# Optimization experiments

Hardware: AMD Instinct MI355X
Metric: run time of the kernel (lower is better)

## Reference

```python
import jax, jax.numpy as jnp
import numpy as np

V = 50257; CTX = 2048; D = 1024; H = 16; L = 8; DH = D // H
B = 2; S = 2048; EPS = 1e-5


def setup_inputs() -> dict:
    key = jax.random.key(0)
    ks = jax.random.split(key, 8)
    s = 0.02
    def n(k, shape):
        return jax.random.normal(k, shape, jnp.float32) * s
    return {
        "x": jax.random.randint(ks[0], (B, S), 0, V),
        "wte": n(ks[1], (V, D)),
        "wpe": n(ks[2], (CTX, D)),
        "ln1_g": jnp.ones((L, D), jnp.float32), "ln1_b": jnp.zeros((L, D), jnp.float32),
        "w_qkv": n(ks[3], (L, D, 3 * D)), "b_qkv": jnp.zeros((L, 3 * D), jnp.float32),
        "w_proj": n(ks[4], (L, D, D)), "b_proj": jnp.zeros((L, D), jnp.float32),
        "ln2_g": jnp.ones((L, D), jnp.float32), "ln2_b": jnp.zeros((L, D), jnp.float32),
        "w_fc": n(ks[5], (L, D, 4 * D)), "b_fc": jnp.zeros((L, 4 * D), jnp.float32),
        "w_cp": n(ks[6], (L, 4 * D, D)), "b_cp": jnp.zeros((L, D), jnp.float32),
        "lnf_g": jnp.ones((D,), jnp.float32), "lnf_b": jnp.zeros((D,), jnp.float32),
        "w_head": n(ks[7], (D, V)),
    }


def layernorm(x, g, b):
    m = x.mean(-1, keepdims=True)
    v = ((x - m) ** 2).mean(-1, keepdims=True)
    return (x - m) * jax.lax.rsqrt(v + EPS) * g + b


def gpt_forward(x, wte, wpe, ln1_g, ln1_b, w_qkv, b_qkv, w_proj, b_proj,
                ln2_g, ln2_b, w_fc, b_fc, w_cp, b_cp, lnf_g, lnf_b, w_head):
    Bx, Sx = x.shape
    h = wte[x] + wpe[:Sx]                       # [B,S,D]
    mask = jnp.tril(jnp.ones((Sx, Sx), bool))   # causal mask
    scale = DH ** -0.5

    def block(h, p):
        g1, b1, wq, bq, wp, bp, g2, b2, wf, bf, wc, bc = p
        y = layernorm(h, g1, b1)
        qkv = y @ wq + bq                        # [B,S,3D]
        q, k, v = jnp.split(qkv, 3, axis=-1)
        q = q.reshape(Bx, Sx, H, DH)
        k = k.reshape(Bx, Sx, H, DH)
        v = v.reshape(Bx, Sx, H, DH)
        att = jnp.einsum('bqhd,bkhd->bhqk', q, k) * scale
        att = jnp.where(mask, att, -jnp.inf)
        att = jax.nn.softmax(att, axis=-1)
        z = jnp.einsum('bhqk,bkhd->bqhd', att, v).reshape(Bx, Sx, D)
        h = h + z @ wp + bp
        y2 = layernorm(h, g2, b2)
        h = h + jax.nn.gelu(y2 @ wf + bf, approximate=False) @ wc + bc
        return h, None

    h, _ = jax.lax.scan(block, h, (ln1_g, ln1_b, w_qkv, b_qkv, w_proj, b_proj,
                                   ln2_g, ln2_b, w_fc, b_fc, w_cp, b_cp))
    h = layernorm(h, lnf_g, lnf_b)
    logits = h[:, -1:, :] @ w_head              # [B,1,V] (last position only)
    return logits


def reference(x, wte, wpe, ln1_g, ln1_b, w_qkv, b_qkv, w_proj, b_proj,
              ln2_g, ln2_b, w_fc, b_fc, w_cp, b_cp, lnf_g, lnf_b, w_head):
    return gpt_forward(x, wte, wpe, ln1_g, ln1_b, w_qkv, b_qkv, w_proj, b_proj,
                       ln2_g, ln2_b, w_fc, b_fc, w_cp, b_cp, lnf_g, lnf_b, w_head)
```

## Files before the change

### kernel.cpp

```cpp
#include <hip/hip_runtime.h>
#include <hip/hip_bf16.h>
#include <math.h>

#define VOCAB 50257
#define CTX 2048
#define DMODEL 1024
#define NHEAD 16
#define NLAYER 8
#define DHEAD 64
#define BATCH 2
#define SEQ 2048
#define NTOK (BATCH * SEQ)

typedef __bf16 bf16x8 __attribute__((ext_vector_type(8)));
typedef float  f32x4  __attribute__((ext_vector_type(4)));
typedef unsigned short ushort4v __attribute__((ext_vector_type(4)));
typedef unsigned short ushort8v __attribute__((ext_vector_type(8)));

__device__ inline void gl_lds16(const void* g, void* l) {
    __builtin_amdgcn_global_load_lds(
        (const __attribute__((address_space(1))) unsigned int*)g,
        (__attribute__((address_space(3))) unsigned int*)l, 16, 0, 0);
}

__device__ inline unsigned short f2bs(float v) {
    __hip_bfloat16 t = __float2bfloat16(v);
    return *(unsigned short*)&t;
}

__global__ void embed_kernel(const int* __restrict__ x,
                             const float* __restrict__ wte,
                             const float* __restrict__ wpe,
                             float* __restrict__ h) {
    int t = blockIdx.x;
    int s = t & (SEQ - 1);
    int tok = x[t];
    const float* pe = wpe + (long)s * DMODEL;
    const float* te = wte + (long)tok * DMODEL;
    float* ph = h + (long)t * DMODEL;
    for (int d = threadIdx.x; d < DMODEL; d += 256)
        ph[d] = te[d] + pe[d];
}

__device__ inline float wave_sum(float v) {
    for (int off = 32; off; off >>= 1) v += __shfl_xor(v, off);
    return v;
}

__device__ void ln_body(char* smem, int row, const float* __restrict__ in,
                        unsigned short* __restrict__ out,
                        const float* __restrict__ g, const float* __restrict__ b) {
    float* red  = (float*)smem;
    float* red2 = red + 4;
    const float* px = in + (long)row * DMODEL;
    unsigned short* po = out + (long)row * DMODEL;
    int tid = threadIdx.x;
    int wid = tid >> 6, lane = tid & 63;

    float x[4];
    float s = 0.f;
    #pragma unroll
    for (int i = 0; i < 4; ++i) { x[i] = px[tid + i * 256]; s += x[i]; }
    s = wave_sum(s);
    if (lane == 0) red[wid] = s;
    __syncthreads();
    float mean = (red[0] + red[1] + red[2] + red[3]) * (1.0f / DMODEL);

    float s2 = 0.f;
    #pragma unroll
    for (int i = 0; i < 4; ++i) { float d = x[i] - mean; s2 += d * d; }
    s2 = wave_sum(s2);
    if (lane == 0) red2[wid] = s2;
    __syncthreads();
    float var = (red2[0] + red2[1] + red2[2] + red2[3]) * (1.0f / DMODEL);
    float r = 1.0f / sqrtf(var + 1e-5f);
    #pragma unroll
    for (int i = 0; i < 4; ++i) {
        int d = tid + i * 256;
        po[d] = f2bs((x[i] - mean) * r * g[d] + b[d]);
    }
}

__global__ void ln_final(const float* __restrict__ in, float* __restrict__ out,
                         const float* __restrict__ g, const float* __restrict__ b,
                         long row_stride) {
    __shared__ float red[4], red2[4];
    int row = blockIdx.x;
    const float* px = in + (long)row * row_stride;
    float* po = out + (long)row * DMODEL;
    int tid = threadIdx.x;
    int wid = tid >> 6, lane = tid & 63;
    float x[4];
    float s = 0.f;
    #pragma unroll
    for (int i = 0; i < 4; ++i) { x[i] = px[tid + i * 256]; s += x[i]; }
    s = wave_sum(s);
    if (lane == 0) red[wid] = s;
    __syncthreads();
    float mean = (red[0] + red[1] + red[2] + red[3]) * (1.0f / DMODEL);
    float s2 = 0.f;
    #pragma unroll
    for (int i = 0; i < 4; ++i) { float d = x[i] - mean; s2 += d * d; }
    s2 = wave_sum(s2);
    if (lane == 0) red2[wid] = s2;
    __syncthreads();
    float var = (red2[0] + red2[1] + red2[2] + red2[3]) * (1.0f / DMODEL);
    float r = 1.0f / sqrtf(var + 1e-5f);
    #pragma unroll
    for (int i = 0; i < 4; ++i) {
        int d = tid + i * 256;
        po[d] = (x[i] - mean) * r * g[d] + b[d];
    }
}

__device__ void convT_body(char* smem, int kx, int ny, const float* __restrict__ W,
                           unsigned short* __restrict__ WT, int K, int N) {
    float (*t)[65] = (float(*)[65])smem;
    const int k0 = kx * 64, n0 = ny * 64;
    const int tid = threadIdx.x;
    {
        const int krow = tid >> 4, c4 = (tid & 15) * 4;
        #pragma unroll
        for (int p = 0; p < 4; ++p) {
            f32x4 gv = *(const f32x4*)&W[(long)(k0 + p * 16 + krow) * N + n0 + c4];
            #pragma unroll
            for (int j = 0; j < 4; ++j) t[p * 16 + krow][c4 + j] = gv[j];
        }
    }
    __syncthreads();
    {
        const int n = tid >> 3, kl = (tid & 7) * 8;
        #pragma unroll
        for (int p = 0; p < 2; ++p) {
            ushort8v pk;
            #pragma unroll
            for (int j = 0; j < 8; ++j) pk[j] = f2bs(t[kl + j][p * 32 + n]);
            *(ushort8v*)&WT[(long)(n0 + p * 32 + n) * K + k0 + kl] = pk;
        }
    }
}

#define STG_A(KS, H) do { \
    const unsigned short* g_ = A + (long)(bm + (H) * 128 + srow) * K + (KS) * 64 + stgch; \
    unsigned short* s_ = LDS + (((KS) & 1) * 2 + (H)) * 8192 + (w * 8) * 64; \
    gl_lds16(g_, s_); gl_lds16(g_ + 64L * K, s_ + 4096); \
} while (0)
#define STG_B(KS, H) do { \
    const unsigned short* g_ = BT + (long)(bn + (H) * 128 + srow) * K + (KS) * 64 + stgch; \
    unsigned short* s_ = LDS + 32768 + (((KS) & 1) * 2 + (H)) * 8192 + (w * 8) * 64; \
    gl_lds16(g_, s_); gl_lds16(g_ + 64L * K, s_ + 4096); \
} while (0)
#define MM2(M_, x0, x1) do { \
    acc[M_][0] = __builtin_amdgcn_mfma_f32_16x16x32_bf16(x0, bfr[0], acc[M_][0], 0, 0, 0); \
    acc[M_][0] = __builtin_amdgcn_mfma_f32_16x16x32_bf16(x1, bfr[1], acc[M_][0], 0, 0, 0); \
    acc[M_][1] = __builtin_amdgcn_mfma_f32_16x16x32_bf16(x0, bfr[2], acc[M_][1], 0, 0, 0); \
    acc[M_][1] = __builtin_amdgcn_mfma_f32_16x16x32_bf16(x1, bfr[3], acc[M_][1], 0, 0, 0); \
    acc[M_][2] = __builtin_amdgcn_mfma_f32_16x16x32_bf16(x0, bfr[4], acc[M_][2], 0, 0, 0); \
    acc[M_][2] = __builtin_amdgcn_mfma_f32_16x16x32_bf16(x1, bfr[5], acc[M_][2], 0, 0, 0); \
    acc[M_][3] = __builtin_amdgcn_mfma_f32_16x16x32_bf16(x0, bfr[6], acc[M_][3], 0, 0, 0); \
    acc[M_][3] = __builtin_amdgcn_mfma_f32_16x16x32_bf16(x1, bfr[7], acc[M_][3], 0, 0, 0); \
} while (0)
#define PHASE(Q, SPAR, STAGE_STMT, TAIL_STMT) do { \
    bf16x8 a00, a01, a10, a11; \
    if (((Q) & 3) == 0) { \
        const unsigned short* Bb_ = lBp[SPAR] + ((wc & 1) * 64 + fr) * 64; \
        bfr[0] = *(const bf16x8*)(Bb_ + rd0);        bfr[1] = *(const bf16x8*)(Bb_ + rd1); \
        bfr[2] = *(const bf16x8*)(Bb_ + 1024 + rd0); bfr[3] = *(const bf16x8*)(Bb_ + 1024 + rd1); \
        bfr[4] = *(const bf16x8*)(Bb_ + 2048 + rd0); bfr[5] = *(const bf16x8*)(Bb_ + 2048 + rd1); \
        bfr[6] = *(const bf16x8*)(Bb_ + 3072 + rd0); bfr[7] = *(const bf16x8*)(Bb_ + 3072 + rd1); \
    } \
    { const unsigned short* Ab_ = lAp[SPAR] + fr * 64; \
      a00 = *(const bf16x8*)(Ab_ + (((Q) & 3) * 2) * 1024 + rd0); \
      a01 = *(const bf16x8*)(Ab_ + (((Q) & 3) * 2) * 1024 + rd1); \
      a10 = *(const bf16x8*)(Ab_ + (((Q) & 3) * 2 + 1) * 1024 + rd0); \
      a11 = *(const bf16x8*)(Ab_ + (((Q) & 3) * 2 + 1) * 1024 + rd1); } \
    STAGE_STMT; \
    __builtin_amdgcn_s_barrier(); \
    asm volatile("s_waitcnt lgkmcnt(0)" ::: "memory"); \
    __builtin_amdgcn_sched_barrier(0); \
    __builtin_amdgcn_s_setprio(1); \
    MM2(((Q) & 3) * 2, a00, a01); \
    MM2(((Q) & 3) * 2 + 1, a10, a11); \
    __builtin_amdgcn_s_setprio(0); \
    TAIL_STMT; \
    __builtin_amdgcn_s_barrier(); \
} while (0)

template<int EPI>
__global__ __launch_bounds__(512, 1)
void mm_mfma256(const unsigned short* __restrict__ A,
                const unsigned short* __restrict__ BT,
                const float* __restrict__ bias,
                void* __restrict__ Cout, int M, int N, int K, int nbx) {
    extern __shared__ unsigned short LDS[];
    const int tid = threadIdx.x;
    const int w = tid >> 6, lane = tid & 63;
    const int wr = w >> 2, wc = w & 3;
    const int nwg = gridDim.x, bid = blockIdx.x;
    const int swz = (bid & 7) * (nwg >> 3) + (bid >> 3);
    const int bm = (swz / nbx) * 256, bn = (swz % nbx) * 256;

    f32x4 acc[8][4];
    #pragma unroll
    for (int m = 0; m < 8; ++m)
        #pragma unroll
        for (int n = 0; n < 4; ++n)
            acc[m][n] = (f32x4){0.f, 0.f, 0.f, 0.f};

    const int fr = lane & 15, kg = lane >> 4;
    const int rd0 = 8 * (kg ^ (lane & 7)), rd1 = 8 * ((kg + 4) ^ (lane & 7));
    const int stgch = 8 * ((lane & 7) ^ (lane >> 3));
    const int srow = w * 8 + (lane >> 3);
    unsigned short* const lAp[2] = { LDS + wr * 8192, LDS + (2 + wr) * 8192 };
    unsigned short* const lBp[2] = { LDS + 32768 + (wc >> 1) * 8192,
                                     LDS + 32768 + (2 + (wc >> 1)) * 8192 };
    bf16x8 bfr[8];

    STG_B(0, 0); STG_B(0, 1); STG_A(0, 0); STG_A(0, 1); STG_B(1, 0); STG_B(1, 1);
    asm volatile("s_waitcnt vmcnt(4)" ::: "memory");
    __builtin_amdgcn_sched_barrier(0);
    __builtin_amdgcn_s_barrier();

    const int T = K >> 7;
    for (int t = 0; t < T; ++t) {
        const int s = 2 * t;
        const bool nl = (t < T - 1);
        PHASE(0, 0, STG_A(s + 1, 0), );
        PHASE(1, 0, STG_A(s + 1, 1), );
        PHASE(2, 0, if (nl) STG_B(s + 2, 0), );
        PHASE(3, 0, if (nl) STG_B(s + 2, 1),
              if (nl) { asm volatile("s_waitcnt vmcnt(4)" ::: "memory"); } else { asm volatile("s_waitcnt vmcnt(0)" ::: "memory"); } __builtin_amdgcn_sched_barrier(0); );
        PHASE(4, 1, if (nl) STG_A(s + 2, 0), );
        PHASE(5, 1, if (nl) STG_A(s + 2, 1), );
        PHASE(6, 1, if (nl) STG_B(s + 3, 0), );
        PHASE(7, 1, if (nl) STG_B(s + 3, 1),
              if (nl) { asm volatile("s_waitcnt vmcnt(4)" ::: "memory"); __builtin_amdgcn_sched_barrier(0); } );
    }

    const int r0 = (lane >> 4) * 4;
    #pragma unroll
    for (int n = 0; n < 4; ++n) {
        int colb = bn + wc * 64 + n * 16;
        float bv = bias[colb + fr];
        #pragma unroll
        for (int m = 0; m < 8; ++m) {
            int rowb = bm + wr * 128 + m * 16 + r0;
            if (EPI == 3) {
                unsigned short* qkvB = (unsigned short*)Cout;
                int which = colb >> 10, hh = (colb & 1023) >> 6, dbase = colb & 63;
                int b_ = rowb >> 11, s_ = rowb & 2047;
                long bh2 = b_ * 16 + hh;
                float v[4];
                #pragma unroll
                for (int r = 0; r < 4; ++r) v[r] = acc[m][n][r] + bv;
                if (which == 2) {
                    ushort4v pk;
                    #pragma unroll
                    for (int r = 0; r < 4; ++r) pk[r] = f2bs(v[r]);
                    *(ushort4v*)&qkvB[8388608L + (bh2 * 64 + dbase + fr) * 2048 + s_] = pk;
                } else {
                    unsigned short* dst = qkvB + (long)which * 4194304L +
                                          (bh2 * 2048 + s_) * 64 + dbase + fr;
                    #pragma unroll
                    for (int r = 0; r < 4; ++r) dst[r * 64] = f2bs(v[r]);
                }
            } else {
                #pragma unroll
                for (int r = 0; r < 4; ++r) {
                    long row = rowb + r, col = colb + fr;
                    float v = acc[m][n][r] + bv;
                    v = 0.5f * v * (1.0f + erff(v * 0.70710678118f));
                    ((__hip_bfloat16*)Cout)[row * N + col] = __float2bfloat16(v);
                }
            }
        }
    }
}

__global__ __launch_bounds__(256)
void mm_mfma_n64(const unsigned short* __restrict__ A,
                 const unsigned short* __restrict__ BT,
                 const float* __restrict__ bias, const float* __restrict__ R,
                 float* __restrict__ Cout, int M, int N, int K) {
    __shared__ unsigned short As[2][128 * 32];
    __shared__ unsigned short Bs[2][64 * 32];
    const int tid = threadIdx.x;
    const int w = tid >> 6, lane = tid & 63;
    const int bm = blockIdx.y * 128, bn = blockIdx.x * 64;
    const int wr = (w >> 1) * 64, wc = (w & 1) * 32;

    f32x4 acc[4][2];
    #pragma unroll
    for (int m = 0; m < 4; ++m)
        #pragma unroll
        for (int n = 0; n < 2; ++n)
            acc[m][n] = (f32x4){0.f, 0.f, 0.f, 0.f};

    const int lrow = lane >> 2;
    const int lcol = (lane & 3) * 8;
    const unsigned short* gA = A + (long)(bm + w * 32 + lrow) * K + lcol;
    const unsigned short* gB = BT + (long)(bn + w * 16 + lrow) * K + lcol;

#define N64_STAGE(K0, BB) do { \
    gl_lds16(gA + (K0),          &As[BB][(w * 32) * 32]); \
    gl_lds16(gA + (K0) + 16 * K, &As[BB][(w * 32 + 16) * 32]); \
    gl_lds16(gB + (K0),          &Bs[BB][(w * 16) * 32]); \
} while (0)

    N64_STAGE(0, 0);
    asm volatile("s_waitcnt vmcnt(0)" ::: "memory");
    __builtin_amdgcn_sched_barrier(0);
    __builtin_amdgcn_s_barrier();

    const int T = K >> 5;
    for (int t = 0; t < T; ++t) {
        const int buf = t & 1;
        if (t + 1 < T) N64_STAGE((t + 1) * 32, buf ^ 1);

        bf16x8 a[4], b[2];
        #pragma unroll
        for (int m = 0; m < 4; ++m)
            a[m] = *(const bf16x8*)&As[buf][(wr + m * 16 + (lane & 15)) * 32 + (lane >> 4) * 8];
        #pragma unroll
        for (int n = 0; n < 2; ++n)
            b[n] = *(const bf16x8*)&Bs[buf][(wc + n * 16 + (lane & 15)) * 32 + (lane >> 4) * 8];
        #pragma unroll
        for (int m = 0; m < 4; ++m)
            #pragma unroll
            for (int n = 0; n < 2; ++n)
                acc[m][n] = __builtin_amdgcn_mfma_f32_16x16x32_bf16(a[m], b[n], acc[m][n], 0, 0, 0);

        asm volatile("s_waitcnt vmcnt(0)" ::: "memory");
        __builtin_amdgcn_sched_barrier(0);
        __builtin_amdgcn_s_barrier();
    }
#undef N64_STAGE

    const int r0 = (lane >> 4) * 4, cc = lane & 15;
    #pragma unroll
    for (int n = 0; n < 2; ++n) {
        int colb = bn + wc + n * 16;
        float bv = bias[colb + cc];
        #pragma unroll
        for (int m = 0; m < 4; ++m) {
            int rowb = bm + wr + m * 16 + r0;
            #pragma unroll
            for (int r = 0; r < 4; ++r) {
                long row = rowb + r, col = colb + cc;
                float v = acc[m][n][r] + bv + R[row * N + col];
                Cout[row * N + col] = v;
            }
        }
    }
}

__device__ void attn_body(char* smem, int bh, int qb,
                          const unsigned short* __restrict__ qB,
                          const unsigned short* __restrict__ kB,
                          const unsigned short* __restrict__ vT,
                          __hip_bfloat16* __restrict__ z) {
    const int tid = threadIdx.x, w = tid >> 6, lane = tid & 63;
    const int arow = lane & 15, kg = lane >> 4;
    unsigned short* Ks = (unsigned short*)smem;
    unsigned short* Vs = Ks + 128 * 64;
    unsigned short* Ps = Vs + 64 * 128 + w * 16 * 128;

    const long kvbase = (long)bh * (2048 * 64);

    bf16x8 qa[2];
    {
        const unsigned short* q0 = qB + kvbase + (long)(qb + w * 16 + arow) * 64 + kg * 8;
        qa[0] = *(const bf16x8*)(q0);
        qa[1] = *(const bf16x8*)(q0 + 32);
    }

    f32x4 po[4];
    float mrow[4], lrow[4];
    #pragma unroll
    for (int i = 0; i < 4; ++i) {
        po[i] = (f32x4){0.f, 0.f, 0.f, 0.f};
        mrow[i] = -1e30f; lrow[i] = 0.f;
    }

    const int ksrow = lane >> 3;
    const int kschunk = (lane & 7) ^ ksrow;
    const int vsr = lane >> 4;
    const int cmax = qb >> 7;

    for (int c = 0; c <= cmax; ++c) {
        {
            const unsigned short* ks0 = kB + kvbase +
                (long)(c * 128 + w * 32 + ksrow) * 64 + kschunk * 8;
            #pragma unroll
            for (int i = 0; i < 4; ++i)
                gl_lds16(ks0 + (long)i * 8 * 64, &Ks[(w * 32 + i * 8) * 64]);
            #pragma unroll
            for (int i = 0; i < 4; ++i) {
                int d = w * 16 + i * 4 + vsr;
                int sch = (lane & 15) ^ (d & 7);
                gl_lds16(vT + kvbase + (long)d * 2048 + c * 128 + sch * 8,
                         &Vs[(w * 16 + i * 4) * 128]);
            }
        }
        __syncthreads();

        f32x4 s[8];
        #pragma unroll
        for (int n = 0; n < 8; ++n) {
            s[n] = (f32x4){0.f, 0.f, 0.f, 0.f};
            int row = n * 16 + arow, sw = row & 7;
            bf16x8 kb0 = *(const bf16x8*)&Ks[row * 64 + (kg ^ sw) * 8];
            bf16x8 kb1 = *(const bf16x8*)&Ks[row * 64 + ((4 + kg) ^ sw) * 8];
            s[n] = __builtin_amdgcn_mfma_f32_16x16x32_bf16(qa[0], kb0, s[n], 0, 0, 0);
            s[n] = __builtin_amdgcn_mfma_f32_16x16x32_bf16(qa[1], kb1, s[n], 0, 0, 0);
        }

        const bool diag = (c == cmax);
        #pragma unroll
        for (int n = 0; n < 8; ++n)
            #pragma unroll
            for (int r = 0; r < 4; ++r) {
                float v = s[n][r] * 0.125f;
                if (diag) {
                    int key = c * 128 + n * 16 + arow;
                    int qrow = qb + w * 16 + kg * 4 + r;
                    if (key > qrow) v = -1e30f;
                }
                s[n][r] = v;
            }

        #pragma unroll
        for (int r = 0; r < 4; ++r) {
            float rm = s[0][r];
            #pragma unroll
            for (int n = 1; n < 8; ++n) rm = fmaxf(rm, s[n][r]);
            #pragma unroll
            for (int off = 1; off < 16; off <<= 1)
                rm = fmaxf(rm, __shfl_xor(rm, off));
            float mnew = fmaxf(mrow[r], rm);
            float esc = expf(mrow[r] - mnew);
            float rs = 0.f;
            #pragma unroll
            for (int n = 0; n < 8; ++n) {
                float p = expf(s[n][r] - mnew);
                s[n][r] = p;
                rs += p;
            }
            #pragma unroll
            for (int off = 1; off < 16; off <<= 1)
                rs += __shfl_xor(rs, off);
            lrow[r] = lrow[r] * esc + rs;
            #pragma unroll
            for (int dt = 0; dt < 4; ++dt) po[dt][r] *= esc;
            mrow[r] = mnew;
        }

        #pragma unroll
        for (int n = 0; n < 8; ++n) {
            int col = n * 16 + arow;
            int chunk = col >> 3, cw = col & 7;
            #pragma unroll
            for (int r = 0; r < 4; ++r) {
                int row = kg * 4 + r;
                Ps[row * 128 + ((chunk ^ (row & 7)) * 8 + cw)] = f2bs(s[n][r]);
            }
        }

        bf16x8 pa[4];
        #pragma unroll
        for (int ks = 0; ks < 4; ++ks)
            pa[ks] = *(const bf16x8*)&Ps[arow * 128 + (((ks * 4 + kg) ^ (arow & 7)) * 8)];
        #pragma unroll
        for (int dt = 0; dt < 4; ++dt) {
            int vrow = dt * 16 + arow, sw = vrow & 7;
            #pragma unroll
            for (int ks = 0; ks < 4; ++ks) {
                bf16x8 vb = *(const bf16x8*)&Vs[vrow * 128 + (((ks * 4 + kg) ^ sw) * 8)];
                po[dt] = __builtin_amdgcn_mfma_f32_16x16x32_bf16(pa[ks], vb, po[dt], 0, 0, 0);
            }
        }
        __syncthreads();
    }

    const int b_ = bh >> 4, hofs = (bh & 15) * 64;
    #pragma unroll
    for (int dt = 0; dt < 4; ++dt)
        #pragma unroll
        for (int r = 0; r < 4; ++r) {
            long row = (long)b_ * 2048 + qb + w * 16 + kg * 4 + r;
            z[row * 1024 + hofs + dt * 16 + arow] = __float2bfloat16(po[dt][r] / lrow[r]);
        }
}

__global__ __launch_bounds__(256)
void fused_ln_convT(const float* __restrict__ h, unsigned short* __restrict__ y,
                    const float* __restrict__ g, const float* __restrict__ b,
                    const float* __restrict__ W, unsigned short* __restrict__ WT,
                    int K, int N, int nLN) {
    extern __shared__ char smem[];
    int bid = blockIdx.x;
    if (bid < nLN) {
        ln_body(smem, bid, h, y, g, b);
    } else {
        int r = bid - nLN, kt = K >> 6;
        convT_body(smem, r % kt, r / kt, W, WT, K, N);
    }
}

__global__ __launch_bounds__(256)
void fused_attn_convT2(const unsigned short* __restrict__ qB,
                       const unsigned short* __restrict__ kB,
                       const unsigned short* __restrict__ vT,
                       __hip_bfloat16* __restrict__ z,
                       const float* __restrict__ W1, unsigned short* __restrict__ WT1,
                       int K1, int N1, int n1,
                       const float* __restrict__ W2, unsigned short* __restrict__ WT2,
                       int K2, int N2, int nAttn) {
    extern __shared__ char smem[];
    int bid = blockIdx.x;
    if (bid < nAttn) {
        attn_body(smem, bid & 31, (bid >> 5) * 64, qB, kB, vT, z);
    } else if (bid < nAttn + n1) {
        int r = bid - nAttn, kt = K1 >> 6;
        convT_body(smem, r % kt, r / kt, W1, WT1, K1, N1);
    } else {
        int r = bid - nAttn - n1, kt = K2 >> 6;
        convT_body(smem, r % kt, r / kt, W2, WT2, K2, N2);
    }
}

__global__ void head_kernel(const float* __restrict__ hl, const float* __restrict__ W,
                            float* __restrict__ out) {
    __shared__ float hs[2 * DMODEL];
    int tid = threadIdx.x;
    #pragma unroll
    for (int i = 0; i < 8; ++i) hs[tid + i * 256] = hl[tid + i * 256];
    __syncthreads();
    int v = blockIdx.x * 256 + tid;
    if (v >= VOCAB) return;
    float a0 = 0.f, a1 = 0.f;
    for (int d = 0; d < DMODEL; ++d) {
        float wv = W[(long)d * VOCAB + v];
        a0 += hs[d] * wv;
        a1 += hs[DMODEL + d] * wv;
    }
    out[v] = a0;
    out[VOCAB + v] = a1;
}

extern "C" void kernel_launch(void* const* d_in, const int* in_sizes, int n_in,
                              void* d_out, int out_size, void* d_ws, size_t ws_size,
                              hipStream_t stream) {
    const int*   x      = (const int*)  d_in[0];
    const float* wte    = (const float*)d_in[1];
    const float* wpe    = (const float*)d_in[2];
    const float* ln1_g  = (const float*)d_in[3];
    const float* ln1_b  = (const float*)d_in[4];
    const float* w_qkv  = (const float*)d_in[5];
    const float* b_qkv  = (const float*)d_in[6];
    const float* w_proj = (const float*)d_in[7];
    const float* b_proj = (const float*)d_in[8];
    const float* ln2_g  = (const float*)d_in[9];
    const float* ln2_b  = (const float*)d_in[10];
    const float* w_fc   = (const float*)d_in[11];
    const float* b_fc   = (const float*)d_in[12];
    const float* w_cp   = (const float*)d_in[13];
    const float* b_cp   = (const float*)d_in[14];
    const float* lnf_g  = (const float*)d_in[15];
    const float* lnf_b  = (const float*)d_in[16];
    const float* w_head = (const float*)d_in[17];
    float* out = (float*)d_out;

    char* ws = (char*)d_ws;
    float*          h     = (float*)ws;
    unsigned short* qkvB  = (unsigned short*)(ws + (16L << 20));
    unsigned short* y_bf  = (unsigned short*)(ws + (40L << 20));
    __hip_bfloat16* z_bf  = (__hip_bfloat16*)(ws + (48L << 20));
    unsigned short* fc_bf = (unsigned short*)(ws + (56L << 20));
    unsigned short* wT_a  = (unsigned short*)(ws + (88L << 20));
    unsigned short* wT_b  = (unsigned short*)(ws + (97L << 20));
    unsigned short* wT_c  = (unsigned short*)(ws + (106L << 20));
    float*          hl    = (float*)(ws + (115L << 20));

    const int SM_CONV = 16640;
    const int SM_ATTN = 49152;

    embed_kernel<<<NTOK, 256, 0, stream>>>(x, wte, wpe, h);

    for (int l = 0; l < NLAYER; ++l) {
        fused_ln_convT<<<4096 + 768, 256, SM_CONV, stream>>>(
            h, y_bf, ln1_g + l * DMODEL, ln1_b + l * DMODEL,
            w_qkv + (long)l * DMODEL * 3072, wT_a, 1024, 3072, 4096);

        mm_mfma256<3><<<192, 512, 131072, stream>>>(
            y_bf, wT_a, b_qkv + l * 3072, qkvB, NTOK, 3072, 1024, 12);

        fused_attn_convT2<<<1024 + 256 + 1024, 256, SM_ATTN, stream>>>(
            qkvB, qkvB + 4194304L, qkvB + 8388608L, z_bf,
            w_proj + (long)l * DMODEL * DMODEL, wT_b, 1024, 1024, 256,
            w_cp + (long)l * 4096 * DMODEL, wT_c, 4096, 1024, 1024);

        mm_mfma_n64<<<dim3(16, 32), 256, 0, stream>>>(
            (const unsigned short*)z_bf, wT_b, b_proj + l * DMODEL, h, h,
            NTOK, 1024, 1024);

        fused_ln_convT<<<4096 + 1024, 256, SM_CONV, stream>>>(
            h, y_bf, ln2_g + l * DMODEL, ln2_b + l * DMODEL,
            w_fc + (long)l * DMODEL * 4096, wT_a, 1024, 4096, 4096);

        mm_mfma256<2><<<256, 512, 131072, stream>>>(
            y_bf, wT_a, b_fc + l * 4096, fc_bf, NTOK, 4096, 1024, 16);

        mm_mfma_n64<<<dim3(16, 32), 256, 0, stream>>>(
            fc_bf, wT_c, b_cp + l * DMODEL, h, h, NTOK, 1024, 4096);
    }

    ln_final<<<BATCH, 256, 0, stream>>>(h + (long)(SEQ - 1) * DMODEL, hl,
                                        lnf_g, lnf_b, (long)SEQ * DMODEL);
    head_kernel<<<(VOCAB + 255) / 256, 256, 0, stream>>>(hl, w_head, out);
}
```

Measured before the change: 2.501 ms.

## Overlap weight conversion with preceding GEMMs instead of layernorm kernels

Weight transpose/convert blocks for the FC weights now ride along with the projection GEMM, and those for the next layer's QKV weights ride along with the c_proj GEMM. The first layer's QKV conversion is fused into the embedding kernel. LayerNorm becomes a standalone kernel. The aim is to fill the idle CUs of the under-occupied 512-block n64 GEMMs with conversion work and shorten the LN launches. The cost is a separate QKV weight buffer and a larger shared-memory footprint for the n64 kernel, since it now uses dynamic smem.

```diff
diff --git a/kernel.cpp b/kernel.cpp
--- a/kernel.cpp
+++ b/kernel.cpp
@@ -28,11 +28,10 @@
     return *(unsigned short*)&t;
 }
 
-__global__ void embed_kernel(const int* __restrict__ x,
-                             const float* __restrict__ wte,
-                             const float* __restrict__ wpe,
-                             float* __restrict__ h) {
-    int t = blockIdx.x;
+__device__ void embed_body(int t, const int* __restrict__ x,
+                           const float* __restrict__ wte,
+                           const float* __restrict__ wpe,
+                           float* __restrict__ h) {
     int s = t & (SEQ - 1);
     int tok = x[t];
     const float* pe = wpe + (long)s * DMODEL;
@@ -47,11 +46,10 @@
     return v;
 }
 
-__device__ void ln_body(char* smem, int row, const float* __restrict__ in,
-                        unsigned short* __restrict__ out,
-                        const float* __restrict__ g, const float* __restrict__ b) {
-    float* red  = (float*)smem;
-    float* red2 = red + 4;
+__global__ void ln_std(const float* __restrict__ in, unsigned short* __restrict__ out,
+                       const float* __restrict__ g, const float* __restrict__ b) {
+    __shared__ float red[4], red2[4];
+    int row = blockIdx.x;
     const float* px = in + (long)row * DMODEL;
     unsigned short* po = out + (long)row * DMODEL;
     int tid = threadIdx.x;
@@ -277,16 +275,16 @@
     }
 }
 
-__global__ __launch_bounds__(256)
-void mm_mfma_n64(const unsigned short* __restrict__ A,
-                 const unsigned short* __restrict__ BT,
-                 const float* __restrict__ bias, const float* __restrict__ R,
-                 float* __restrict__ Cout, int M, int N, int K) {
-    __shared__ unsigned short As[2][128 * 32];
-    __shared__ unsigned short Bs[2][64 * 32];
+__device__ void n64_body(char* smem, int bx, int by,
+                         const unsigned short* __restrict__ A,
+                         const unsigned short* __restrict__ BT,
+                         const float* __restrict__ bias, const float* __restrict__ R,
+                         float* __restrict__ Cout, int M, int N, int K) {
+    unsigned short* As = (unsigned short*)smem;
+    unsigned short* Bs = As + 2 * 128 * 32;
     const int tid = threadIdx.x;
     const int w = tid >> 6, lane = tid & 63;
-    const int bm = blockIdx.y * 128, bn = blockIdx.x * 64;
+    const int bm = by * 128, bn = bx * 64;
     const int wr = (w >> 1) * 64, wc = (w & 1) * 32;
 
     f32x4 acc[4][2];
@@ -302,9 +300,9 @@
     const unsigned short* gB = BT + (long)(bn + w * 16 + lrow) * K + lcol;
 
 #define N64_STAGE(K0, BB) do { \
-    gl_lds16(gA + (K0),          &As[BB][(w * 32) * 32]); \
-    gl_lds16(gA + (K0) + 16 * K, &As[BB][(w * 32 + 16) * 32]); \
-    gl_lds16(gB + (K0),          &Bs[BB][(w * 16) * 32]); \
+    gl_lds16(gA + (K0),          &As[(BB) * 4096 + (w * 32) * 32]); \
+    gl_lds16(gA + (K0) + 16 * K, &As[(BB) * 4096 + (w * 32 + 16) * 32]); \
+    gl_lds16(gB + (K0),          &Bs[(BB) * 2048 + (w * 16) * 32]); \
 } while (0)
 
     N64_STAGE(0, 0);
@@ -320,10 +318,10 @@
         bf16x8 a[4], b[2];
         #pragma unroll
         for (int m = 0; m < 4; ++m)
-            a[m] = *(const bf16x8*)&As[buf][(wr + m * 16 + (lane & 15)) * 32 + (lane >> 4) * 8];
+            a[m] = *(const bf16x8*)&As[buf * 4096 + (wr + m * 16 + (lane & 15)) * 32 + (lane >> 4) * 8];
         #pragma unroll
         for (int n = 0; n < 2; ++n)
-            b[n] = *(const bf16x8*)&Bs[buf][(wc + n * 16 + (lane & 15)) * 32 + (lane >> 4) * 8];
+            b[n] = *(const bf16x8*)&Bs[buf * 2048 + (wc + n * 16 + (lane & 15)) * 32 + (lane >> 4) * 8];
         #pragma unroll
         for (int m = 0; m < 4; ++m)
             #pragma unroll
@@ -493,16 +491,16 @@
 }
 
 __global__ __launch_bounds__(256)
-void fused_ln_convT(const float* __restrict__ h, unsigned short* __restrict__ y,
-                    const float* __restrict__ g, const float* __restrict__ b,
-                    const float* __restrict__ W, unsigned short* __restrict__ WT,
-                    int K, int N, int nLN) {
+void fused_embed_convT(const int* __restrict__ x, const float* __restrict__ wte,
+                       const float* __restrict__ wpe, float* __restrict__ h,
+                       const float* __restrict__ W, unsigned short* __restrict__ WT,
+                       int K, int N, int nEmb) {
     extern __shared__ char smem[];
     int bid = blockIdx.x;
-    if (bid < nLN) {
-        ln_body(smem, bid, h, y, g, b);
+    if (bid < nEmb) {
+        embed_body(bid, x, wte, wpe, h);
     } else {
-        int r = bid - nLN, kt = K >> 6;
+        int r = bid - nEmb, kt = K >> 6;
         convT_body(smem, r % kt, r / kt, W, WT, K, N);
     }
 }
@@ -525,6 +523,23 @@
         convT_body(smem, r % kt, r / kt, W1, WT1, K1, N1);
     } else {
         int r = bid - nAttn - n1, kt = K2 >> 6;
+        convT_body(smem, r % kt, r / kt, W2, WT2, K2, N2);
+    }
+}
+
+__global__ __launch_bounds__(256)
+void fused_n64_convT(const unsigned short* __restrict__ A,
+                     const unsigned short* __restrict__ BT,
+                     const float* __restrict__ bias, const float* __restrict__ R,
+                     float* __restrict__ Cout, int M, int N, int K, int nbx,
+                     const float* __restrict__ W2, unsigned short* __restrict__ WT2,
+                     int K2, int N2, int nMM) {
+    extern __shared__ char smem[];
+    int bid = blockIdx.x;
+    if (bid < nMM) {
+        n64_body(smem, bid % nbx, bid / nbx, A, BT, bias, R, Cout, M, N, K);
+    } else {
+        int r = bid - nMM, kt = K2 >> 6;
         convT_body(smem, r % kt, r / kt, W2, WT2, K2, N2);
     }
 }
@@ -580,39 +595,41 @@
     unsigned short* wT_a  = (unsigned short*)(ws + (88L << 20));
     unsigned short* wT_b  = (unsigned short*)(ws + (97L << 20));
     unsigned short* wT_c  = (unsigned short*)(ws + (106L << 20));
-    float*          hl    = (float*)(ws + (115L << 20));
+    unsigned short* wT_q  = (unsigned short*)(ws + (115L << 20));
+    float*          hl    = (float*)(ws + (124L << 20));
 
     const int SM_CONV = 16640;
     const int SM_ATTN = 49152;
-
-    embed_kernel<<<NTOK, 256, 0, stream>>>(x, wte, wpe, h);
+    const int SM_N64  = 24576;
+
+    fused_embed_convT<<<4096 + 768, 256, SM_CONV, stream>>>(
+        x, wte, wpe, h, w_qkv, wT_q, 1024, 3072, 4096);
 
     for (int l = 0; l < NLAYER; ++l) {
-        fused_ln_convT<<<4096 + 768, 256, SM_CONV, stream>>>(
-            h, y_bf, ln1_g + l * DMODEL, ln1_b + l * DMODEL,
-            w_qkv + (long)l * DMODEL * 3072, wT_a, 1024, 3072, 4096);
+        ln_std<<<NTOK, 256, 0, stream>>>(h, y_bf, ln1_g + l * DMODEL, ln1_b + l * DMODEL);
 
         mm_mfma256<3><<<192, 512, 131072, stream>>>(
-            y_bf, wT_a, b_qkv + l * 3072, qkvB, NTOK, 3072, 1024, 12);
+            y_bf, wT_q, b_qkv + l * 3072, qkvB, NTOK, 3072, 1024, 12);
 
         fused_attn_convT2<<<1024 + 256 + 1024, 256, SM_ATTN, stream>>>(
             qkvB, qkvB + 4194304L, qkvB + 8388608L, z_bf,
             w_proj + (long)l * DMODEL * DMODEL, wT_b, 1024, 1024, 256,
             w_cp + (long)l * 4096 * DMODEL, wT_c, 4096, 1024, 1024);
 
-        mm_mfma_n64<<<dim3(16, 32), 256, 0, stream>>>(
+        fused_n64_convT<<<512 + 1024, 256, SM_N64, stream>>>(
             (const unsigned short*)z_bf, wT_b, b_proj + l * DMODEL, h, h,
-            NTOK, 1024, 1024);
-
-        fused_ln_convT<<<4096 + 1024, 256, SM_CONV, stream>>>(
-            h, y_bf, ln2_g + l * DMODEL, ln2_b + l * DMODEL,
-            w_fc + (long)l * DMODEL * 4096, wT_a, 1024, 4096, 4096);
+            NTOK, 1024, 1024, 16,
+            w_fc + (long)l * DMODEL * 4096, wT_a, 1024, 4096, 512);
+
+        ln_std<<<NTOK, 256, 0, stream>>>(h, y_bf, ln2_g + l * DMODEL, ln2_b + l * DMODEL);
 
         mm_mfma256<2><<<256, 512, 131072, stream>>>(
             y_bf, wT_a, b_fc + l * 4096, fc_bf, NTOK, 4096, 1024, 16);
 
-        mm_mfma_n64<<<dim3(16, 32), 256, 0, stream>>>(
-            fc_bf, wT_c, b_cp + l * DMODEL, h, h, NTOK, 1024, 4096);
+        int nConv = (l + 1 < NLAYER) ? 768 : 0;
+        fused_n64_convT<<<512 + nConv, 256, SM_N64, stream>>>(
+            fc_bf, wT_c, b_cp + l * DMODEL, h, h, NTOK, 1024, 4096, 16,
+            w_qkv + (long)(l + 1) * DMODEL * 3072, wT_q, 1024, 3072, 512);
     }
 
     ln_final<<<BATCH, 256, 0, stream>>>(h + (long)(SEQ - 1) * DMODEL, hl,
```

Result: faster. 2.426 ms (-3.0%).
